# Kernel optimization log

Hardware: AMD Instinct MI355X
Metric: run time of the kernel (lower is better)

Reference implementation:

```python
import jax, jax.numpy as jnp
import numpy as np

N = 100000   # nodes
E = 625000   # edges
D = 128      # input feature dim
H = 128      # hidden_channels
L = 2        # num_layers
NEG = 0.2    # leaky relu negative slope
BN_EPS = 1e-5


def setup_inputs() -> dict:
    key = jax.random.key(0)
    ks = jax.random.split(key, 12)
    s = 0.05
    return {
        "x": jax.random.normal(ks[0], (N, D), jnp.float32),
        "edge_index": jax.random.randint(ks[1], (2, E), 0, N, dtype=jnp.int32),
        "Wl": jax.random.normal(ks[2], (L, D, H), jnp.float32) * s,   # GATv2 lin_l (source)
        "bl": jax.random.normal(ks[3], (L, H), jnp.float32) * s,
        "Wr": jax.random.normal(ks[4], (L, D, H), jnp.float32) * s,   # GATv2 lin_r (target)
        "br": jax.random.normal(ks[5], (L, H), jnp.float32) * s,
        "att": jax.random.normal(ks[6], (L, H), jnp.float32) * s,     # attention vector a
        "cb": jax.random.normal(ks[7], (L, H), jnp.float32) * s,      # conv output bias
        "Wlin": jax.random.normal(ks[8], (L, H, H), jnp.float32) * s, # extra Linear
        "blin": jax.random.normal(ks[9], (L, H), jnp.float32) * s,
        "gamma": jnp.ones((L, H), jnp.float32),                       # BatchNorm weight
        "beta": jnp.zeros((L, H), jnp.float32),                       # BatchNorm bias
    }


def reference(x, edge_index, Wl, bl, Wr, br, att, cb, Wlin, blin, gamma, beta):
    src, dst = edge_index[0], edge_index[1]
    for i in range(L):
        # GATv2Conv (1 head, no self-loops)
        xs = x @ Wl[i] + bl[i]                 # [N, H] source transform
        xd = x @ Wr[i] + br[i]                 # [N, H] target transform
        e = jax.nn.leaky_relu(xs[src] + xd[dst], NEG)   # [E, H]
        logits = e @ att[i]                    # [E]
        m = jax.ops.segment_max(logits, dst, num_segments=N)
        a = jnp.exp(logits - m[dst])
        denom = jax.ops.segment_sum(a, dst, num_segments=N) + 1e-16
        alpha = a / denom[dst]                 # scatter-softmax over dst
        out = jax.ops.segment_sum(alpha[:, None] * xs[src], dst, num_segments=N) + cb[i]
        # x += lin(x)
        out = out + out @ Wlin[i] + blin[i]
        # BatchNorm1d (training mode: batch stats, biased var)
        mu = out.mean(axis=0)
        var = out.var(axis=0)
        x = (out - mu) * jax.lax.rsqrt(var + BN_EPS) * gamma[i] + beta[i]
        if i < L - 1:
            x = jax.nn.relu(x)
    return x
```

## Files before the change

### kernel.cpp

```cpp
#include <hip/hip_runtime.h>

#define NN 100000
#define NE 625000
#define HD 128

typedef unsigned int u32;
typedef unsigned short u16;
typedef __bf16 bf16x8 __attribute__((ext_vector_type(8)));
typedef float f32x4 __attribute__((ext_vector_type(4)));
typedef float f32x2 __attribute__((ext_vector_type(2)));

__device__ __forceinline__ u16 f2b(float f) {
  u32 u = __float_as_uint(f);
  u32 r = (u + 0x7FFFu + ((u >> 16) & 1u)) >> 16;
  return (u16)r;
}
__device__ __forceinline__ float b2f(u32 u) { return __uint_as_float(u << 16); }

__global__ void k_prep_w(const float* __restrict__ Wl, const float* __restrict__ Wr,
                         const float* __restrict__ Wlin, u16* __restrict__ Wt) {
  int i = blockIdx.x * blockDim.x + threadIdx.x;
  if (i >= 6 * 16384) return;
  int mat = i >> 14;
  int l = mat / 3, which = mat % 3;
  int rem = i & 16383;
  int hh = rem >> 7, dd = rem & 127;
  const float* src = (which == 0) ? Wl : (which == 1) ? Wr : Wlin;
  float v = src[l * 16384 + dd * 128 + hh];
  if (which == 2 && dd == hh) v += 1.0f;
  Wt[l * (3 * 16384) + which * 16384 + hh * 128 + dd] = f2b(v);
}

__global__ void k_cast_x(const float* __restrict__ x, u16* __restrict__ xb) {
  int i = blockIdx.x * blockDim.x + threadIdx.x;
  if (i >= NN * 32) return;
  float4 v = *(const float4*)(x + i * 4);
  uint2 o;
  o.x = (u32)f2b(v.x) | ((u32)f2b(v.y) << 16);
  o.y = (u32)f2b(v.z) | ((u32)f2b(v.w) << 16);
  *(uint2*)(xb + i * 4) = o;
}

__global__ void k_hist(const int* __restrict__ dst, int* __restrict__ deg) {
  int e = blockIdx.x * blockDim.x + threadIdx.x;
  if (e < NE) atomicAdd(&deg[dst[e]], 1);
}

__global__ void k_alloc(const int* __restrict__ deg, int* __restrict__ row_start,
                        int* __restrict__ cursor) {
  int idx = blockIdx.x * blockDim.x + threadIdx.x;
  int lane = threadIdx.x & 63;
  int v = (idx < NN) ? deg[idx] : 0;
  int incl = v;
  #pragma unroll
  for (int off = 1; off < 64; off <<= 1) {
    int t = __shfl_up(incl, off, 64);
    if (lane >= off) incl += t;
  }
  int total = __shfl(incl, 63, 64);
  int base = 0;
  if (lane == 63) base = atomicAdd(cursor, total);
  base = __shfl(base, 63, 64);
  if (idx < NN) row_start[idx] = base + incl - v;
}

__global__ void k_fill(const int* __restrict__ src, const int* __restrict__ dst,
                       const int* __restrict__ row_start, int* __restrict__ cnt,
                       int* __restrict__ ss) {
  int e = blockIdx.x * blockDim.x + threadIdx.x;
  if (e >= NE) return;
  int d = dst[e];
  int p = row_start[d] + atomicAdd(&cnt[d], 1);
  ss[p] = src[e];
}

__global__ __launch_bounds__(256) void k_gemm4(
    const u16* __restrict__ A, const u16* __restrict__ Bt0, const u16* __restrict__ Bt1,
    const float* __restrict__ bias0, const float* __restrict__ bias1,
    u16* __restrict__ o0, u16* __restrict__ o1,
    const float* __restrict__ bn_sum, const float* __restrict__ bn_sq,
    const float* __restrict__ bn_g, const float* __restrict__ bn_b,
    float* __restrict__ st_sum, float* __restrict__ st_sq, int nB) {
  __shared__ __align__(16) u16 lA[128 * 136];
  __shared__ __align__(16) u16 lB[64 * 136];
  const int tid = threadIdx.x;
  const int m0 = blockIdx.x * 128;
  const int rr = tid >> 4;
  const int seg = tid & 15;

  float mu[8], sc[8], bb[8];
  if (bn_sum) {
    const float invn = 1.0f / 100000.0f;
    #pragma unroll
    for (int j = 0; j < 8; ++j) {
      int c = seg * 8 + j;
      float m = bn_sum[c] * invn;
      float v = fmaxf(bn_sq[c] * invn - m * m, 0.f);
      mu[j] = m;
      sc[j] = rsqrtf(v + 1e-5f) * bn_g[c];
      bb[j] = bn_b[c];
    }
  }
  #pragma unroll
  for (int p = 0; p < 8; ++p) {
    int row = p * 16 + rr;
    int g = m0 + row;
    int gc = (g < NN) ? g : (NN - 1);
    uint4 v = *(const uint4*)(A + gc * HD + seg * 8);
    if (bn_sum) {
      u32 w[4] = {v.x, v.y, v.z, v.w};
      #pragma unroll
      for (int k = 0; k < 4; ++k) {
        float lo = fmaxf((b2f(w[k] & 0xFFFFu) - mu[2 * k]) * sc[2 * k] + bb[2 * k], 0.f);
        float hi = fmaxf((b2f(w[k] >> 16) - mu[2 * k + 1]) * sc[2 * k + 1] + bb[2 * k + 1], 0.f);
        w[k] = (u32)f2b(lo) | ((u32)f2b(hi) << 16);
      }
      v.x = w[0]; v.y = w[1]; v.z = w[2]; v.w = w[3];
    }
    *(uint4*)(lA + row * 136 + seg * 8) = v;
  }
  #pragma unroll
  for (int p = 0; p < 4; ++p) {
    int n = p * 16 + rr;
    uint4 v = *(const uint4*)(Bt0 + n * HD + seg * 8);
    *(uint4*)(lB + n * 136 + seg * 8) = v;
  }
  __syncthreads();

  const int wv = tid >> 6;
  const int lane = tid & 63;
  const int colt = lane & 15;
  const int kq = lane >> 4;
  const int rq = kq * 4;
  bf16x8 af[2][4];
  #pragma unroll
  for (int tile = 0; tile < 2; ++tile)
    #pragma unroll
    for (int s = 0; s < 4; ++s)
      af[tile][s] = *(const bf16x8*)(lA + ((wv * 2 + tile) * 16 + colt) * 136 + s * 32 + kq * 8);

  for (int pass = 0; pass < nB; ++pass) {
    const u16* Bt = pass ? Bt1 : Bt0;
    u16* o = pass ? o1 : o0;
    const float* bias = pass ? bias1 : bias0;
    if (pass == 1) {
      __syncthreads();
      #pragma unroll
      for (int p = 0; p < 4; ++p) {
        int n = p * 16 + rr;
        uint4 v = *(const uint4*)(Bt + n * HD + seg * 8);
        *(uint4*)(lB + n * 136 + seg * 8) = v;
      }
      __syncthreads();
    }
    #pragma unroll
    for (int half = 0; half < 2; ++half) {
      if (half == 1) {
        __syncthreads();
        #pragma unroll
        for (int p = 0; p < 4; ++p) {
          int n = p * 16 + rr;
          uint4 v = *(const uint4*)(Bt + (64 + n) * HD + seg * 8);
          *(uint4*)(lB + n * 136 + seg * 8) = v;
        }
        __syncthreads();
      }
      #pragma unroll
      for (int tt = 0; tt < 4; ++tt) {
        int t = half * 4 + tt;
        bf16x8 bf[4];
        #pragma unroll
        for (int s = 0; s < 4; ++s)
          bf[s] = *(const bf16x8*)(lB + (tt * 16 + colt) * 136 + s * 32 + kq * 8);
        const int c = t * 16 + colt;
        const float bs = bias[c];
        #pragma unroll
        for (int tile = 0; tile < 2; ++tile) {
          f32x4 acc = {0.f, 0.f, 0.f, 0.f};
          #pragma unroll
          for (int s = 0; s < 4; ++s)
            acc = __builtin_amdgcn_mfma_f32_16x16x32_bf16(af[tile][s], bf[s], acc, 0, 0, 0);
          #pragma unroll
          for (int r = 0; r < 4; ++r)
            lA[((wv * 2 + tile) * 16 + rq + r) * 136 + c] = f2b(acc[r] + bs);
        }
      }
    }
    __syncthreads();
    float s8[8], q8[8];
    #pragma unroll
    for (int j = 0; j < 8; ++j) { s8[j] = 0.f; q8[j] = 0.f; }
    #pragma unroll
    for (int i = 0; i < 8; ++i) {
      int row = i * 16 + rr;
      int g = m0 + row;
      if (g < NN) {
        uint4 v = *(const uint4*)(lA + row * 136 + seg * 8);
        *(uint4*)(o + g * HD + seg * 8) = v;
        if (st_sum && pass == 0) {
          u32 w[4] = {v.x, v.y, v.z, v.w};
          #pragma unroll
          for (int k = 0; k < 4; ++k) {
            float lo = b2f(w[k] & 0xFFFFu), hi = b2f(w[k] >> 16);
            s8[2 * k] += lo; q8[2 * k] += lo * lo;
            s8[2 * k + 1] += hi; q8[2 * k + 1] += hi * hi;
          }
        }
      }
    }
    if (st_sum && pass == 0) {
      __syncthreads();
      float* red = (float*)lB;
      #pragma unroll
      for (int j = 0; j < 8; ++j) {
        red[rr * 128 + seg * 8 + j] = s8[j];
        red[2048 + rr * 128 + seg * 8 + j] = q8[j];
      }
      __syncthreads();
      if (tid < 128) {
        float S = 0.f, Q = 0.f;
        #pragma unroll
        for (int u = 0; u < 16; ++u) {
          S += red[u * 128 + tid];
          Q += red[2048 + u * 128 + tid];
        }
        atomicAdd(&st_sum[tid], S);
        atomicAdd(&st_sq[tid], Q);
      }
    }
  }
}

__global__ __launch_bounds__(256) void k_edge3(
    const u16* __restrict__ xs_b, const u16* __restrict__ xd_b,
    const int* __restrict__ row_start, const int* __restrict__ deg,
    const int* __restrict__ ss, const float* __restrict__ att,
    const float* __restrict__ cb, u16* __restrict__ out_b) {
  int dv = blockIdx.x * 4 + (threadIdx.x >> 6);
  if (dv >= NN) return;
  int lane = threadIdx.x & 63;
  float2 av = *(const float2*)(att + 2 * lane);
  const float L2E = 1.4426950408889634f;
  f32x2 a6 = {L2E * 0.6f * av.x, L2E * 0.6f * av.y};
  f32x2 a4 = {L2E * 0.4f * av.x, L2E * 0.4f * av.y};
  u32 xdp = ((const u32*)xd_b)[dv * 64 + lane];
  f32x2 xd2 = {b2f(xdp & 0xFFFFu), b2f(xdp >> 16)};
  int base = row_start[dv], n = deg[dv];
  const u32* xs32 = (const u32*)xs_b;
  f32x2 acc = {0.f, 0.f};
  float wsum = 0.f;
  for (int e0 = 0; e0 < n; e0 += 4) {
    int idx[4];
    #pragma unroll
    for (int j = 0; j < 4; ++j) {
      int e = e0 + j;
      idx[j] = ss[base + ((e < n) ? e : 0)];
    }
    f32x2 xv[4];
    #pragma unroll
    for (int j = 0; j < 4; ++j) {
      u32 p = xs32[idx[j] * 64 + lane];
      f32x2 t = {b2f(p & 0xFFFFu), b2f(p >> 16)};
      xv[j] = t;
    }
    float q[4];
    #pragma unroll
    for (int j = 0; j < 4; ++j) {
      f32x2 t = xv[j] + xd2;
      f32x2 ab = {__builtin_fabsf(t.x), __builtin_fabsf(t.y)};
      f32x2 qv = a4 * ab + a6 * t;
      q[j] = qv.x + qv.y;
    }
    float sA0 = (lane & 1) ? q[1] : q[0];
    float oA0 = (lane & 1) ? q[0] : q[1];
    sA0 += __shfl_xor(oA0, 1, 64);
    float sA1 = (lane & 1) ? q[3] : q[2];
    float oA1 = (lane & 1) ? q[2] : q[3];
    sA1 += __shfl_xor(oA1, 1, 64);
    float sC = (lane & 2) ? sA1 : sA0;
    float oC = (lane & 2) ? sA0 : sA1;
    sC += __shfl_xor(oC, 2, 64);
    sC += __shfl_xor(sC, 4, 64);
    sC += __shfl_xor(sC, 8, 64);
    sC += __shfl_xor(sC, 16, 64);
    sC += __shfl_xor(sC, 32, 64);
    float eE = exp2f(sC);
    float w0 = __shfl(eE, 0, 64);
    float w1 = __shfl(eE, 1, 64);
    float w2 = __shfl(eE, 2, 64);
    float w3 = __shfl(eE, 3, 64);
    w1 = (e0 + 1 < n) ? w1 : 0.f;
    w2 = (e0 + 2 < n) ? w2 : 0.f;
    w3 = (e0 + 3 < n) ? w3 : 0.f;
    wsum += (w0 + w1) + (w2 + w3);
    acc += xv[0] * w0;
    acc += xv[1] * w1;
    acc += xv[2] * w2;
    acc += xv[3] * w3;
  }
  float inv = 1.f / (wsum + 1e-16f);
  float2 cbv = *(const float2*)(cb + 2 * lane);
  float o0 = acc.x * inv + cbv.x;
  float o1 = acc.y * inv + cbv.y;
  ((u32*)out_b)[dv * 64 + lane] = (u32)f2b(o0) | ((u32)f2b(o1) << 16);
}

__global__ void k_bn(const u16* __restrict__ hb, const float* __restrict__ ssum,
                     const float* __restrict__ ssq, const float* __restrict__ gamma,
                     const float* __restrict__ beta, float* __restrict__ fout) {
  int i = blockIdx.x * blockDim.x + threadIdx.x;
  if (i >= NN * 64) return;
  int cp = (i & 63) * 2;
  u32 xp = ((const u32*)hb)[i];
  float v0 = b2f(xp & 0xFFFFu), v1 = b2f(xp >> 16);
  const float invn = 1.0f / 100000.0f;
  float mu0 = ssum[cp] * invn, mu1 = ssum[cp + 1] * invn;
  float va0 = fmaxf(ssq[cp] * invn - mu0 * mu0, 0.f);
  float va1 = fmaxf(ssq[cp + 1] * invn - mu1 * mu1, 0.f);
  float s0 = rsqrtf(va0 + 1e-5f) * gamma[cp];
  float s1 = rsqrtf(va1 + 1e-5f) * gamma[cp + 1];
  float o0 = (v0 - mu0) * s0 + beta[cp];
  float o1 = (v1 - mu1) * s1 + beta[cp + 1];
  int row = i >> 6;
  *(float2*)(fout + row * 128 + cp) = make_float2(o0, o1);
}

extern "C" void kernel_launch(void* const* d_in, const int* in_sizes, int n_in,
                              void* d_out, int out_size, void* d_ws, size_t ws_size,
                              hipStream_t stream) {
  const float* x    = (const float*)d_in[0];
  const int*   ei   = (const int*)d_in[1];
  const float* Wl   = (const float*)d_in[2];
  const float* bl   = (const float*)d_in[3];
  const float* Wr   = (const float*)d_in[4];
  const float* br   = (const float*)d_in[5];
  const float* att  = (const float*)d_in[6];
  const float* cb   = (const float*)d_in[7];
  const float* Wlin = (const float*)d_in[8];
  const float* blin = (const float*)d_in[9];
  const float* gm   = (const float*)d_in[10];
  const float* bt   = (const float*)d_in[11];
  const int* esrc = ei;
  const int* edst = ei + NE;

  u16* xb    = (u16*)d_ws;
  u16* xs_b  = xb + NN * HD;
  u16* xd_b  = xs_b + NN * HD;
  u16* out_b = xd_b + NN * HD;
  u16* Wt    = out_b + NN * HD;
  int* deg       = (int*)(Wt + 6 * 16384);
  int* cnt       = deg + NN;
  int* cursor    = cnt + NN;
  int* row_start = cursor + 1;
  int* srcs      = row_start + NN;
  float* ssum0   = (float*)(srcs + NE);
  float* ssq0    = ssum0 + 128;
  float* ssum1   = ssq0 + 128;
  float* ssq1    = ssum1 + 128;

  hipMemsetAsync(deg, 0, (size_t)(2 * NN + 1) * 4, stream);
  hipMemsetAsync(ssum0, 0, 4 * 128 * 4, stream);
  k_prep_w<<<(6 * 16384 + 255) / 256, 256, 0, stream>>>(Wl, Wr, Wlin, Wt);
  k_cast_x<<<(NN * 32 + 255) / 256, 256, 0, stream>>>(x, xb);
  k_hist<<<(NE + 255) / 256, 256, 0, stream>>>(edst, deg);
  k_alloc<<<(NN + 255) / 256, 256, 0, stream>>>(deg, row_start, cursor);
  k_fill<<<(NE + 255) / 256, 256, 0, stream>>>(esrc, edst, row_start, cnt, srcs);

  const int gg = (NN + 127) / 128;
  const u16* wt0_l = Wt;             const u16* wt0_r = Wt + 16384;     const u16* wt0_lin = Wt + 2 * 16384;
  const u16* wt1_l = Wt + 3 * 16384; const u16* wt1_r = Wt + 4 * 16384; const u16* wt1_lin = Wt + 5 * 16384;

  k_gemm4<<<gg, 256, 0, stream>>>(xb, wt0_l, wt0_r, bl, br, xs_b, xd_b,
                                  nullptr, nullptr, nullptr, nullptr,
                                  nullptr, nullptr, 2);
  k_edge3<<<(NN + 3) / 4, 256, 0, stream>>>(xs_b, xd_b, row_start, deg, srcs,
                                            att, cb, out_b);
  k_gemm4<<<gg, 256, 0, stream>>>(out_b, wt0_lin, nullptr, blin, nullptr,
                                  out_b, nullptr,
                                  nullptr, nullptr, nullptr, nullptr,
                                  ssum0, ssq0, 1);
  k_gemm4<<<gg, 256, 0, stream>>>(out_b, wt1_l, wt1_r, bl + 128, br + 128,
                                  xs_b, xd_b,
                                  ssum0, ssq0, gm, bt,
                                  nullptr, nullptr, 2);
  k_edge3<<<(NN + 3) / 4, 256, 0, stream>>>(xs_b, xd_b, row_start, deg, srcs,
                                            att + 128, cb + 128, out_b);
  k_gemm4<<<gg, 256, 0, stream>>>(out_b, wt1_lin, nullptr, blin + 128, nullptr,
                                  out_b, nullptr,
                                  nullptr, nullptr, nullptr, nullptr,
                                  ssum1, ssq1, 1);
  k_bn<<<(NN * 64 + 255) / 256, 256, 0, stream>>>(out_b, ssum1, ssq1,
                                                  gm + 128, bt + 128, (float*)d_out);
}
```

Baseline: 462.6 us.

## Split wavefront into four 16-lane edge groups with 16-byte row gathers

The edge aggregation kernel now assigns each 16-lane quarter of a wavefront to a different edge. Each lane loads 8 bf16 features with one 16-byte load, so a wavefront gathers four source rows in parallel instead of looping over them with 4-byte loads. The attention dot-product reduction shrinks to a 16-lane DPP row reduction, replacing the full 64-lane shuffle tree and the weight broadcasts. Partial accumulators from the four groups are combined with cross-group shuffles at the end, and only the first group writes the output. This trades more accumulator registers and a final reduction for wider memory transactions and fewer shuffles per edge.

```diff
diff --git a/kernel.cpp b/kernel.cpp
--- a/kernel.cpp
+++ b/kernel.cpp
@@ -16,6 +16,12 @@
   return (u16)r;
 }
 __device__ __forceinline__ float b2f(u32 u) { return __uint_as_float(u << 16); }
+
+template <int CTRL>
+__device__ __forceinline__ float dppadd(float x) {
+  int t = __builtin_amdgcn_update_dpp(0, __float_as_int(x), CTRL, 0xf, 0xf, true);
+  return x + __int_as_float(t);
+}
 
 __global__ void k_prep_w(const float* __restrict__ Wl, const float* __restrict__ Wr,
                          const float* __restrict__ Wlin, u16* __restrict__ Wt) {
@@ -231,78 +237,96 @@
   }
 }
 
-__global__ __launch_bounds__(256) void k_edge3(
+__global__ __launch_bounds__(256) void k_edge4(
     const u16* __restrict__ xs_b, const u16* __restrict__ xd_b,
     const int* __restrict__ row_start, const int* __restrict__ deg,
     const int* __restrict__ ss, const float* __restrict__ att,
     const float* __restrict__ cb, u16* __restrict__ out_b) {
   int dv = blockIdx.x * 4 + (threadIdx.x >> 6);
   if (dv >= NN) return;
-  int lane = threadIdx.x & 63;
-  float2 av = *(const float2*)(att + 2 * lane);
+  const int lane = threadIdx.x & 63;
+  const int cl = lane & 15;
+  const int grp = lane >> 4;
+
   const float L2E = 1.4426950408889634f;
-  f32x2 a6 = {L2E * 0.6f * av.x, L2E * 0.6f * av.y};
-  f32x2 a4 = {L2E * 0.4f * av.x, L2E * 0.4f * av.y};
-  u32 xdp = ((const u32*)xd_b)[dv * 64 + lane];
-  f32x2 xd2 = {b2f(xdp & 0xFFFFu), b2f(xdp >> 16)};
-  int base = row_start[dv], n = deg[dv];
-  const u32* xs32 = (const u32*)xs_b;
-  f32x2 acc = {0.f, 0.f};
+  float4 av0 = *(const float4*)(att + cl * 8);
+  float4 av1 = *(const float4*)(att + cl * 8 + 4);
+  float al[8] = {av0.x, av0.y, av0.z, av0.w, av1.x, av1.y, av1.z, av1.w};
+  f32x2 a6[4], a4[4];
+  #pragma unroll
+  for (int k = 0; k < 4; ++k) {
+    a6[k].x = L2E * 0.6f * al[2 * k];     a6[k].y = L2E * 0.6f * al[2 * k + 1];
+    a4[k].x = L2E * 0.4f * al[2 * k];     a4[k].y = L2E * 0.4f * al[2 * k + 1];
+  }
+  uint4 xdp = *(const uint4*)(xd_b + dv * HD + cl * 8);
+  u32 xdw[4] = {xdp.x, xdp.y, xdp.z, xdp.w};
+  f32x2 xd4[4];
+  #pragma unroll
+  for (int k = 0; k < 4; ++k) {
+    xd4[k].x = __uint_as_float(xdw[k] << 16);
+    xd4[k].y = __uint_as_float(xdw[k] & 0xFFFF0000u);
+  }
+
+  const int base = row_start[dv];
+  const int n = deg[dv];
+  f32x2 acc[4] = {{0.f, 0.f}, {0.f, 0.f}, {0.f, 0.f}, {0.f, 0.f}};
   float wsum = 0.f;
+
   for (int e0 = 0; e0 < n; e0 += 4) {
-    int idx[4];
-    #pragma unroll
-    for (int j = 0; j < 4; ++j) {
-      int e = e0 + j;
-      idx[j] = ss[base + ((e < n) ? e : 0)];
-    }
+    int e = e0 + grp;
+    int idx = ss[base + ((e < n) ? e : 0)];
+    uint4 p = *(const uint4*)(xs_b + idx * HD + cl * 8);
+    u32 pw[4] = {p.x, p.y, p.z, p.w};
     f32x2 xv[4];
-    #pragma unroll
-    for (int j = 0; j < 4; ++j) {
-      u32 p = xs32[idx[j] * 64 + lane];
-      f32x2 t = {b2f(p & 0xFFFFu), b2f(p >> 16)};
-      xv[j] = t;
-    }
-    float q[4];
-    #pragma unroll
-    for (int j = 0; j < 4; ++j) {
-      f32x2 t = xv[j] + xd2;
+    f32x2 qv = {0.f, 0.f};
+    #pragma unroll
+    for (int k = 0; k < 4; ++k) {
+      f32x2 x2;
+      x2.x = __uint_as_float(pw[k] << 16);
+      x2.y = __uint_as_float(pw[k] & 0xFFFF0000u);
+      xv[k] = x2;
+      f32x2 t = x2 + xd4[k];
       f32x2 ab = {__builtin_fabsf(t.x), __builtin_fabsf(t.y)};
-      f32x2 qv = a4 * ab + a6 * t;
-      q[j] = qv.x + qv.y;
-    }
-    float sA0 = (lane & 1) ? q[1] : q[0];
-    float oA0 = (lane & 1) ? q[0] : q[1];
-    sA0 += __shfl_xor(oA0, 1, 64);
-    float sA1 = (lane & 1) ? q[3] : q[2];
-    float oA1 = (lane & 1) ? q[2] : q[3];
-    sA1 += __shfl_xor(oA1, 1, 64);
-    float sC = (lane & 2) ? sA1 : sA0;
-    float oC = (lane & 2) ? sA0 : sA1;
-    sC += __shfl_xor(oC, 2, 64);
-    sC += __shfl_xor(sC, 4, 64);
-    sC += __shfl_xor(sC, 8, 64);
-    sC += __shfl_xor(sC, 16, 64);
-    sC += __shfl_xor(sC, 32, 64);
-    float eE = exp2f(sC);
-    float w0 = __shfl(eE, 0, 64);
-    float w1 = __shfl(eE, 1, 64);
-    float w2 = __shfl(eE, 2, 64);
-    float w3 = __shfl(eE, 3, 64);
-    w1 = (e0 + 1 < n) ? w1 : 0.f;
-    w2 = (e0 + 2 < n) ? w2 : 0.f;
-    w3 = (e0 + 3 < n) ? w3 : 0.f;
-    wsum += (w0 + w1) + (w2 + w3);
-    acc += xv[0] * w0;
-    acc += xv[1] * w1;
-    acc += xv[2] * w2;
-    acc += xv[3] * w3;
-  }
-  float inv = 1.f / (wsum + 1e-16f);
-  float2 cbv = *(const float2*)(cb + 2 * lane);
-  float o0 = acc.x * inv + cbv.x;
-  float o1 = acc.y * inv + cbv.y;
-  ((u32*)out_b)[dv * 64 + lane] = (u32)f2b(o0) | ((u32)f2b(o1) << 16);
+      qv += a4[k] * ab;
+      qv += a6[k] * t;
+    }
+    float q = qv.x + qv.y;
+    q = dppadd<0xB1>(q);
+    q = dppadd<0x4E>(q);
+    q = dppadd<0x124>(q);
+    q = dppadd<0x128>(q);
+    float w = (e < n) ? exp2f(q) : 0.f;
+    wsum += w;
+    #pragma unroll
+    for (int k = 0; k < 4; ++k) acc[k] += xv[k] * w;
+  }
+
+  #pragma unroll
+  for (int k = 0; k < 4; ++k) {
+    acc[k].x += __shfl_xor(acc[k].x, 16, 64);
+    acc[k].y += __shfl_xor(acc[k].y, 16, 64);
+    acc[k].x += __shfl_xor(acc[k].x, 32, 64);
+    acc[k].y += __shfl_xor(acc[k].y, 32, 64);
+  }
+  wsum += __shfl_xor(wsum, 16, 64);
+  wsum += __shfl_xor(wsum, 32, 64);
+
+  if (grp == 0) {
+    float inv = 1.f / (wsum + 1e-16f);
+    float4 cb0 = *(const float4*)(cb + cl * 8);
+    float4 cb1 = *(const float4*)(cb + cl * 8 + 4);
+    float cbl[8] = {cb0.x, cb0.y, cb0.z, cb0.w, cb1.x, cb1.y, cb1.z, cb1.w};
+    u32 ow[4];
+    #pragma unroll
+    for (int k = 0; k < 4; ++k) {
+      float o0 = acc[k].x * inv + cbl[2 * k];
+      float o1 = acc[k].y * inv + cbl[2 * k + 1];
+      ow[k] = (u32)f2b(o0) | ((u32)f2b(o1) << 16);
+    }
+    uint4 o;
+    o.x = ow[0]; o.y = ow[1]; o.z = ow[2]; o.w = ow[3];
+    *(uint4*)(out_b + dv * HD + cl * 8) = o;
+  }
 }
 
 __global__ void k_bn(const u16* __restrict__ hb, const float* __restrict__ ssum,
@@ -373,7 +397,7 @@
   k_gemm4<<<gg, 256, 0, stream>>>(xb, wt0_l, wt0_r, bl, br, xs_b, xd_b,
                                   nullptr, nullptr, nullptr, nullptr,
                                   nullptr, nullptr, 2);
-  k_edge3<<<(NN + 3) / 4, 256, 0, stream>>>(xs_b, xd_b, row_start, deg, srcs,
+  k_edge4<<<(NN + 3) / 4, 256, 0, stream>>>(xs_b, xd_b, row_start, deg, srcs,
                                             att, cb, out_b);
   k_gemm4<<<gg, 256, 0, stream>>>(out_b, wt0_lin, nullptr, blin, nullptr,
                                   out_b, nullptr,
@@ -383,7 +407,7 @@
                                   xs_b, xd_b,
                                   ssum0, ssq0, gm, bt,
                                   nullptr, nullptr, 2);
-  k_edge3<<<(NN + 3) / 4, 256, 0, stream>>>(xs_b, xd_b, row_start, deg, srcs,
+  k_edge4<<<(NN + 3) / 4, 256, 0, stream>>>(xs_b, xd_b, row_start, deg, srcs,
                                             att + 128, cb + 128, out_b);
   k_gemm4<<<gg, 256, 0, stream>>>(out_b, wt1_lin, nullptr, blin + 128, nullptr,
                                   out_b, nullptr,
```

After: 457.4 us. About the same (-1.1%).
